# Performance work log

Hardware: AMD Instinct MI355X
Metric: run time of the kernel (lower is better)

Reference implementation:

```python
import jax, jax.numpy as jnp
import numpy as np

GT_POSITIVE_THRESHOLD = 3.0  # pixels, from config['gt_positive_threshold']


def setup_inputs() -> dict:
    key = jax.random.key(0)
    k0, k1, k2 = jax.random.split(key, 3)
    B, N0, N1 = 8, 2048, 2048
    W, H = 640.0, 480.0
    scale = jnp.array([W, H], dtype=jnp.float32)
    kpts0 = jax.random.uniform(k0, (B, N0, 2), dtype=jnp.float32) * scale
    kpts1 = jax.random.uniform(k1, (B, N1, 2), dtype=jnp.float32) * scale
    # near-identity homography per pair (small perturbation keeps points in-frame)
    transformation = (jnp.eye(3, dtype=jnp.float32)[None]
                      + 0.001 * jax.random.normal(k2, (B, 3, 3), dtype=jnp.float32))
    return {"kpts0": kpts0, "kpts1": kpts1, "transformation": transformation}


def _reproject_keypoints(kpts, H):
    # kpts: [B,N,2], H: [B,3,3] homography. Homogeneous projection.
    ones = jnp.ones(kpts.shape[:-1] + (1,), dtype=kpts.dtype)
    pts_h = jnp.concatenate([kpts, ones], axis=-1)           # [B,N,3]
    proj = jnp.einsum('bij,bnj->bni', H, pts_h)              # [B,N,3]
    return proj[..., :2] / (proj[..., 2:3] + 1e-8)


def _cdist(a, b):
    # a: [B,N0,2], b: [B,N1,2] -> [B,N0,N1] Euclidean distances
    a2 = jnp.sum(a * a, axis=-1)                             # [B,N0]
    b2 = jnp.sum(b * b, axis=-1)                             # [B,N1]
    ab = jnp.einsum('bnd,bmd->bnm', a, b)                    # [B,N0,N1]
    d2 = a2[:, :, None] + b2[:, None, :] - 2.0 * ab
    return jnp.sqrt(jnp.maximum(d2, 0.0))


def reference(kpts0, kpts1, transformation):
    B, N0, _ = kpts0.shape
    N1 = kpts1.shape[1]
    kpts0_t = _reproject_keypoints(kpts0, transformation)
    err = _cdist(kpts0_t, kpts1)                             # [B,N0,N1]

    min_dist0 = jnp.min(err, axis=2)                         # [B,N0]
    gt_matches0 = jnp.argmin(err, axis=2).astype(jnp.int32)  # [B,N0]
    gt_matches1 = jnp.argmin(err, axis=1).astype(jnp.int32)  # [B,N1]

    # cross-check: kpts1's best match of kpts0's best match must be the kpt itself
    back = jnp.take_along_axis(gt_matches1, gt_matches0, axis=1)  # [B,N0]
    idx0 = jnp.arange(N0, dtype=jnp.int32)[None, :]
    inconsistent = (back != idx0) | (min_dist0 > GT_POSITIVE_THRESHOLD)
    gt_matches0 = jnp.where(inconsistent, -1, gt_matches0)

    # rebuild inverse map: gt_matches1[b, gt_matches0[b,i]] = i for valid i
    valid = gt_matches0 != -1
    tgt = jnp.where(valid, gt_matches0, N1)                  # N1 is out-of-range -> dropped
    src = jnp.broadcast_to(idx0, (B, N0))
    gt_matches1_out = jnp.full((B, N1), -1, dtype=jnp.int32)
    gt_matches1_out = gt_matches1_out.at[jnp.arange(B)[:, None], tgt].set(src, mode='drop')

    return gt_matches0, gt_matches1_out, min_dist0
```

## Files before the change

### kernel.cpp

```cpp
#include <hip/hip_runtime.h>


#define SPN 2048
#define SPT 16384
#define HGRID (SPT / 16)

__device__ __forceinline__ void sp_reproject(const float* __restrict__ T, int b,
                                             float x, float y,
                                             float& X, float& Y, float& S) {
  const float* H = T + b * 9;
  float p0 = __fadd_rn(__fadd_rn(__fmul_rn(H[0], x), __fmul_rn(H[1], y)), H[2]);
  float p1 = __fadd_rn(__fadd_rn(__fmul_rn(H[3], x), __fmul_rn(H[4], y)), H[5]);
  float p2 = __fadd_rn(__fadd_rn(__fmul_rn(H[6], x), __fmul_rn(H[7], y)), H[8]);
  float den = __fadd_rn(p2, 1e-8f);
  X = __fdiv_rn(p0, den);
  Y = __fdiv_rn(p1, den);
  S = __fadd_rn(__fmul_rn(X, X), __fmul_rn(Y, Y));
}

__global__ __launch_bounds__(256) void sp_prep(
    const float2* __restrict__ k0, const float2* __restrict__ k1,
    const float* __restrict__ T, float4* __restrict__ q0, float4* __restrict__ q1) {
  int t = blockIdx.x * 256 + threadIdx.x;
  if (t < SPT) {
    float2 p = k0[t];
    float X, Y, S;
    sp_reproject(T, t >> 11, p.x, p.y, X, Y, S);
    q0[t] = make_float4(X, Y, S, 0.0f);
  } else {
    int u = t - SPT;
    float2 p = k1[u];
    float S = __fadd_rn(__fmul_rn(p.x, p.x), __fmul_rn(p.y, p.y));
    q1[u] = make_float4(p.x, p.y, S, 0.0f);
  }
}

__global__ __launch_bounds__(256, 4) void SuperPointMatchesGenerator_56925496541369_kernel(
    const float4* __restrict__ q0, const float4* __restrict__ q1,
    unsigned short* __restrict__ gt0p, unsigned short* __restrict__ gt1,
    float* __restrict__ out_mind) {
  __shared__ float4 cand[SPN];
  const int tid = threadIdx.x;
  const bool m1 = blockIdx.x >= HGRID;
  const int base = (m1 ? blockIdx.x - HGRID : blockIdx.x) << 4;
  const int b = base >> 11, cb = b << 11;
  const float4* __restrict__ qr = m1 ? q1 : q0;
  const float4* __restrict__ qc = (m1 ? q0 : q1) + cb;

  float4 stage[8];
#pragma unroll
  for (int k = 0; k < 8; k++) stage[k] = qc[(k << 8) + tid];
#pragma unroll
  for (int k = 0; k < 8; k++) cand[(k << 8) + tid] = stage[k];

  float rx2[16], ry2[16], rsv[16], bv[16];
  int bi[16];
#pragma unroll
  for (int r = 0; r < 16; r++) {
    float4 v = qr[base + r];
    rx2[r] = __fmul_rn(2.0f, v.x);
    ry2[r] = __fmul_rn(2.0f, v.y);
    rsv[r] = v.z;
    bv[r] = INFINITY; bi[r] = 0;
  }
  __syncthreads();

  float4 vv[8];
#pragma unroll
  for (int k = 0; k < 8; k++) vv[k] = cand[(k << 8) + tid];
#pragma unroll
  for (int k = 0; k < 8; k++) {
    const int c = (k << 8) + tid;
#pragma unroll
    for (int r = 0; r < 16; r++) {
      float tw = __fadd_rn(__fmul_rn(rx2[r], vv[k].x), __fmul_rn(ry2[r], vv[k].y));
      float s  = __fadd_rn(rsv[r], vv[k].z);
      float d2 = __fsub_rn(s, tw);
      if (d2 < bv[r]) { bv[r] = d2; bi[r] = c; }
    }
  }
  __syncthreads();

  unsigned long long* keys = (unsigned long long*)cand;
#pragma unroll
  for (int r = 0; r < 16; r++) {
    float dm = fmaxf(bv[r], 0.0f);
    keys[(r << 8) + tid] =
        ((unsigned long long)__float_as_uint(dm) << 32) | (unsigned)bi[r];
  }
  __syncthreads();

  const int wv = tid >> 6, ln = tid & 63;
#pragma unroll
  for (int rr = 0; rr < 4; rr++) {
    const int r = (wv << 2) + rr;
    unsigned long long k0 = keys[(r << 8) + ln];
    unsigned long long t;
    t = keys[(r << 8) + 64 + ln];  if (t < k0) k0 = t;
    t = keys[(r << 8) + 128 + ln]; if (t < k0) k0 = t;
    t = keys[(r << 8) + 192 + ln]; if (t < k0) k0 = t;
#pragma unroll
    for (int off = 32; off > 0; off >>= 1) {
      unsigned long long o = __shfl_down(k0, off);
      if (o < k0) k0 = o;
    }
    if (ln == 0) {
      int idx = (int)(k0 & 0x7ffu);
      if (!m1) {
        float e = __fsqrt_rn(__uint_as_float((unsigned)(k0 >> 32)));
        unsigned short pk = (unsigned short)idx;
        if (e > 3.0f) pk |= 0x8000u;
        gt0p[base + r] = pk;
        out_mind[base + r] = e;
      } else {
        gt1[base + r] = (unsigned short)idx;
      }
    }
  }
}

__global__ __launch_bounds__(256) void SuperPointMatchesGenerator_56925496541369_final(
    const unsigned short* __restrict__ gt0p, const unsigned short* __restrict__ gt1,
    float* __restrict__ out) {
  int t = blockIdx.x * 256 + threadIdx.x;
  if (t >= SPT) return;
  int b = t >> 11, i = t & 2047, cb = b << 11;

  unsigned short p0 = gt0p[t];
  int m0 = p0 & 0x7ff;
  bool ok0 = ((p0 & 0x8000u) == 0) && ((int)gt1[cb + m0] == i);
  out[t] = ok0 ? (float)m0 : -1.0f;

  int istar = gt1[t];
  unsigned short ps = gt0p[cb + istar];
  bool ok1 = (((int)(ps & 0x7ff)) == i) && ((ps & 0x8000u) == 0);
  out[SPT + t] = ok1 ? (float)istar : -1.0f;
}

__global__ __launch_bounds__(256) void sp_fb_main(
    const float2* __restrict__ k0, const float2* __restrict__ k1,
    const float* __restrict__ T, unsigned short* __restrict__ gt0p,
    unsigned short* __restrict__ gt1, float* __restrict__ out_mind) {
  const bool mode1 = blockIdx.x >= SPN;
  const int base = (mode1 ? blockIdx.x - SPN : blockIdx.x) * 8;
  const int b = base >> 11, cb = b << 11;
  float rx[8], ry[8], rs[8], bv[8];
  int bi[8];
#pragma unroll
  for (int r = 0; r < 8; r++) { bv[r] = INFINITY; bi[r] = 0; }
  if (!mode1) {
#pragma unroll
    for (int r = 0; r < 8; r++) {
      float2 p = k0[base + r];
      sp_reproject(T, b, p.x, p.y, rx[r], ry[r], rs[r]);
    }
    for (int c = threadIdx.x; c < SPN; c += 256) {
      float2 p = k1[cb + c];
      float b2 = __fadd_rn(__fmul_rn(p.x, p.x), __fmul_rn(p.y, p.y));
#pragma unroll
      for (int r = 0; r < 8; r++) {
        float ab = __fadd_rn(__fmul_rn(rx[r], p.x), __fmul_rn(ry[r], p.y));
        float d2 = __fsub_rn(__fadd_rn(rs[r], b2), __fmul_rn(2.0f, ab));
        float dm = fmaxf(d2, 0.0f);
        if (dm < bv[r]) { bv[r] = dm; bi[r] = c; }
      }
    }
  } else {
#pragma unroll
    for (int r = 0; r < 8; r++) {
      float2 p = k1[base + r];
      rx[r] = p.x; ry[r] = p.y;
      rs[r] = __fadd_rn(__fmul_rn(p.x, p.x), __fmul_rn(p.y, p.y));
    }
    for (int c = threadIdx.x; c < SPN; c += 256) {
      float2 p = k0[cb + c];
      float cx, cy, a2;
      sp_reproject(T, b, p.x, p.y, cx, cy, a2);
#pragma unroll
      for (int r = 0; r < 8; r++) {
        float ab = __fadd_rn(__fmul_rn(rx[r], cx), __fmul_rn(ry[r], cy));
        float d2 = __fsub_rn(__fadd_rn(a2, rs[r]), __fmul_rn(2.0f, ab));
        float dm = fmaxf(d2, 0.0f);
        if (dm < bv[r]) { bv[r] = dm; bi[r] = c; }
      }
    }
  }
  unsigned long long key[8];
#pragma unroll
  for (int r = 0; r < 8; r++)
    key[r] = ((unsigned long long)__float_as_uint(bv[r]) << 32) | (unsigned)bi[r];
#pragma unroll
  for (int off = 32; off > 0; off >>= 1) {
#pragma unroll
    for (int r = 0; r < 8; r++) {
      unsigned long long o = __shfl_down(key[r], off);
      if (o < key[r]) key[r] = o;
    }
  }
  __shared__ unsigned long long part[4][8];
  if ((threadIdx.x & 63) == 0) {
    int w = threadIdx.x >> 6;
#pragma unroll
    for (int r = 0; r < 8; r++) part[w][r] = key[r];
  }
  __syncthreads();
  if (threadIdx.x < 8) {
    int r = threadIdx.x;
    unsigned long long k = part[0][r];
#pragma unroll
    for (int w = 1; w < 4; w++)
      if (part[w][r] < k) k = part[w][r];
    int idx = (int)(k & 0x7ffu);
    if (!mode1) {
      float e = __fsqrt_rn(__uint_as_float((unsigned)(k >> 32)));
      unsigned short pk = (unsigned short)idx;
      if (e > 3.0f) pk |= 0x8000u;
      gt0p[base + r] = pk;
      out_mind[base + r] = e;
    } else {
      gt1[base + r] = (unsigned short)idx;
    }
  }
}

extern "C" void kernel_launch(void* const* d_in, const int* in_sizes, int n_in,
                              void* d_out, int out_size, void* d_ws, size_t ws_size,
                              hipStream_t stream) {
  (void)in_sizes; (void)n_in; (void)out_size;
  const float2* k0 = (const float2*)d_in[0];
  const float2* k1 = (const float2*)d_in[1];
  const float* T   = (const float*)d_in[2];
  float* out = (float*)d_out;

  const size_t need = (size_t)2 * SPT * sizeof(float4) + (size_t)2 * SPT * sizeof(unsigned short);
  if (ws_size >= need) {
    float4* q0 = (float4*)d_ws;
    float4* q1 = q0 + SPT;
    unsigned short* gt0p = (unsigned short*)(q1 + SPT);
    unsigned short* gt1  = gt0p + SPT;
    sp_prep<<<2 * SPT / 256, 256, 0, stream>>>(k0, k1, T, q0, q1);
    SuperPointMatchesGenerator_56925496541369_kernel<<<2 * HGRID, 256, 0, stream>>>(
        q0, q1, gt0p, gt1, out + 2 * SPT);
    SuperPointMatchesGenerator_56925496541369_final<<<SPT / 256, 256, 0, stream>>>(
        gt0p, gt1, out);
  } else {
    unsigned short* gt0p = (unsigned short*)d_ws;
    unsigned short* gt1  = gt0p + SPT;
    sp_fb_main<<<2 * SPN, 256, 0, stream>>>(k0, k1, T, gt0p, gt1, out + 2 * SPT);
    SuperPointMatchesGenerator_56925496541369_final<<<SPT / 256, 256, 0, stream>>>(
        gt0p, gt1, out);
  }
}
```

Baseline: 79.35 us.

## Fuse prep, argmin and cross-check into one cooperative kernel with grid syncs

Replaces the three-kernel sequence (prep, bidirectional argmin, final cross-check) with a single cooperative kernel of 1024 blocks. Grid-wide syncs separate the phases, and each block handles both directions in turn. The aim is to remove two kernel launch gaps. In exchange it relies on cooperative launch support and the cost of grid.sync, and the grid is half as wide per phase, which may lower parallelism. The multi-kernel path is kept as a fallback, and the old no-workspace path is removed.

```diff
diff --git a/kernel.cpp b/kernel.cpp
--- a/kernel.cpp
+++ b/kernel.cpp
@@ -1,8 +1,12 @@
 #include <hip/hip_runtime.h>
+#include <hip/hip_cooperative_groups.h>
+
+namespace cg = cooperative_groups;
 
 
 #define SPN 2048
 #define SPT 16384
+#define CGRID 1024
 #define HGRID (SPT / 16)
 
 __device__ __forceinline__ void sp_reproject(const float* __restrict__ T, int b,
@@ -16,6 +20,127 @@
   X = __fdiv_rn(p0, den);
   Y = __fdiv_rn(p1, den);
   S = __fadd_rn(__fmul_rn(X, X), __fmul_rn(Y, Y));
+}
+
+__global__ __launch_bounds__(256, 4) void SuperPointMatchesGenerator_56925496541369_kernel(
+    const float2* __restrict__ k0, const float2* __restrict__ k1,
+    const float* __restrict__ T, float4* __restrict__ q0, float4* __restrict__ q1,
+    unsigned short* __restrict__ gt0p, unsigned short* __restrict__ gt1,
+    float* __restrict__ out) {
+  cg::grid_group grid = cg::this_grid();
+  __shared__ float4 cand[SPN + 512];
+  const int tid = threadIdx.x;
+  const int gt = (int)blockIdx.x * 256 + tid;
+  float* __restrict__ out_mind = out + 2 * SPT;
+
+  if (gt < 2 * SPT) {
+    if (gt < SPT) {
+      float2 p = k0[gt];
+      float X, Y, S;
+      sp_reproject(T, gt >> 11, p.x, p.y, X, Y, S);
+      q0[gt] = make_float4(X, Y, S, 0.0f);
+    } else {
+      int u = gt - SPT;
+      float2 p = k1[u];
+      float S = __fadd_rn(__fmul_rn(p.x, p.x), __fmul_rn(p.y, p.y));
+      q1[u] = make_float4(p.x, p.y, S, 0.0f);
+    }
+  }
+  grid.sync();
+
+  for (int half = 0; half < 2; half++) {
+    __syncthreads();
+    const bool m1 = (half == 1);
+    const int base = (int)blockIdx.x << 4;
+    const int b = base >> 11, cb = b << 11;
+    const float4* __restrict__ qr = m1 ? q1 : q0;
+    const float4* __restrict__ qc = (m1 ? q0 : q1) + cb;
+
+    float4 stage[8];
+#pragma unroll
+    for (int k = 0; k < 8; k++) stage[k] = qc[(k << 8) + tid];
+#pragma unroll
+    for (int k = 0; k < 8; k++) cand[(k << 8) + tid] = stage[k];
+
+    float rx2[16], ry2[16], rsv[16], bv[16];
+    int bi[16];
+#pragma unroll
+    for (int r = 0; r < 16; r++) {
+      float4 v = qr[base + r];
+      rx2[r] = __fmul_rn(2.0f, v.x);
+      ry2[r] = __fmul_rn(2.0f, v.y);
+      rsv[r] = v.z;
+      bv[r] = INFINITY; bi[r] = 0;
+    }
+    __syncthreads();
+
+    float4 vv[8];
+#pragma unroll
+    for (int k = 0; k < 8; k++) vv[k] = cand[(k << 8) + tid];
+#pragma unroll
+    for (int k = 0; k < 8; k++) {
+      const int c = (k << 8) + tid;
+#pragma unroll
+      for (int r = 0; r < 16; r++) {
+        float tw = __fadd_rn(__fmul_rn(rx2[r], vv[k].x), __fmul_rn(ry2[r], vv[k].y));
+        float s  = __fadd_rn(rsv[r], vv[k].z);
+        float d2 = __fsub_rn(s, tw);
+        if (d2 < bv[r]) { bv[r] = d2; bi[r] = c; }
+      }
+    }
+    __syncthreads();
+
+    unsigned long long* keys = (unsigned long long*)cand;
+#pragma unroll
+    for (int r = 0; r < 16; r++) {
+      float dm = fmaxf(bv[r], 0.0f);
+      keys[(r << 8) + tid] =
+          ((unsigned long long)__float_as_uint(dm) << 32) | (unsigned)bi[r];
+    }
+    __syncthreads();
+
+    const int wv = tid >> 6, ln = tid & 63;
+#pragma unroll
+    for (int rr = 0; rr < 4; rr++) {
+      const int r = (wv << 2) + rr;
+      unsigned long long kk = keys[(r << 8) + ln];
+      unsigned long long t;
+      t = keys[(r << 8) + 64 + ln];  if (t < kk) kk = t;
+      t = keys[(r << 8) + 128 + ln]; if (t < kk) kk = t;
+      t = keys[(r << 8) + 192 + ln]; if (t < kk) kk = t;
+#pragma unroll
+      for (int off = 32; off > 0; off >>= 1) {
+        unsigned long long o = __shfl_down(kk, off);
+        if (o < kk) kk = o;
+      }
+      if (ln == 0) {
+        int idx = (int)(kk & 0x7ffu);
+        if (!m1) {
+          float e = __fsqrt_rn(__uint_as_float((unsigned)(kk >> 32)));
+          unsigned short pk = (unsigned short)idx;
+          if (e > 3.0f) pk |= 0x8000u;
+          gt0p[base + r] = pk;
+          out_mind[base + r] = e;
+        } else {
+          gt1[base + r] = (unsigned short)idx;
+        }
+      }
+    }
+  }
+  grid.sync();
+
+  if (gt < SPT) {
+    int b2 = gt >> 11, i = gt & 2047, cb2 = b2 << 11;
+    unsigned short p0 = gt0p[gt];
+    int m0i = p0 & 0x7ff;
+    bool ok0 = ((p0 & 0x8000u) == 0) && ((int)gt1[cb2 + m0i] == i);
+    out[gt] = ok0 ? (float)m0i : -1.0f;
+
+    int istar = gt1[gt];
+    unsigned short ps = gt0p[cb2 + istar];
+    bool ok1 = (((int)(ps & 0x7ff)) == i) && ((ps & 0x8000u) == 0);
+    out[SPT + gt] = ok1 ? (float)istar : -1.0f;
+  }
 }
 
 __global__ __launch_bounds__(256) void sp_prep(
@@ -35,7 +160,7 @@
   }
 }
 
-__global__ __launch_bounds__(256, 4) void SuperPointMatchesGenerator_56925496541369_kernel(
+__global__ __launch_bounds__(256, 4) void sp_main3(
     const float4* __restrict__ q0, const float4* __restrict__ q1,
     unsigned short* __restrict__ gt0p, unsigned short* __restrict__ gt1,
     float* __restrict__ out_mind) {
@@ -94,20 +219,20 @@
 #pragma unroll
   for (int rr = 0; rr < 4; rr++) {
     const int r = (wv << 2) + rr;
-    unsigned long long k0 = keys[(r << 8) + ln];
+    unsigned long long kk = keys[(r << 8) + ln];
     unsigned long long t;
-    t = keys[(r << 8) + 64 + ln];  if (t < k0) k0 = t;
-    t = keys[(r << 8) + 128 + ln]; if (t < k0) k0 = t;
-    t = keys[(r << 8) + 192 + ln]; if (t < k0) k0 = t;
+    t = keys[(r << 8) + 64 + ln];  if (t < kk) kk = t;
+    t = keys[(r << 8) + 128 + ln]; if (t < kk) kk = t;
+    t = keys[(r << 8) + 192 + ln]; if (t < kk) kk = t;
 #pragma unroll
     for (int off = 32; off > 0; off >>= 1) {
-      unsigned long long o = __shfl_down(k0, off);
-      if (o < k0) k0 = o;
+      unsigned long long o = __shfl_down(kk, off);
+      if (o < kk) kk = o;
     }
     if (ln == 0) {
-      int idx = (int)(k0 & 0x7ffu);
+      int idx = (int)(kk & 0x7ffu);
       if (!m1) {
-        float e = __fsqrt_rn(__uint_as_float((unsigned)(k0 >> 32)));
+        float e = __fsqrt_rn(__uint_as_float((unsigned)(kk >> 32)));
         unsigned short pk = (unsigned short)idx;
         if (e > 3.0f) pk |= 0x8000u;
         gt0p[base + r] = pk;
@@ -119,7 +244,7 @@
   }
 }
 
-__global__ __launch_bounds__(256) void SuperPointMatchesGenerator_56925496541369_final(
+__global__ __launch_bounds__(256) void sp_final3(
     const unsigned short* __restrict__ gt0p, const unsigned short* __restrict__ gt1,
     float* __restrict__ out) {
   int t = blockIdx.x * 256 + threadIdx.x;
@@ -137,117 +262,42 @@
   out[SPT + t] = ok1 ? (float)istar : -1.0f;
 }
 
-__global__ __launch_bounds__(256) void sp_fb_main(
-    const float2* __restrict__ k0, const float2* __restrict__ k1,
-    const float* __restrict__ T, unsigned short* __restrict__ gt0p,
-    unsigned short* __restrict__ gt1, float* __restrict__ out_mind) {
-  const bool mode1 = blockIdx.x >= SPN;
-  const int base = (mode1 ? blockIdx.x - SPN : blockIdx.x) * 8;
-  const int b = base >> 11, cb = b << 11;
-  float rx[8], ry[8], rs[8], bv[8];
-  int bi[8];
-#pragma unroll
-  for (int r = 0; r < 8; r++) { bv[r] = INFINITY; bi[r] = 0; }
-  if (!mode1) {
-#pragma unroll
-    for (int r = 0; r < 8; r++) {
-      float2 p = k0[base + r];
-      sp_reproject(T, b, p.x, p.y, rx[r], ry[r], rs[r]);
-    }
-    for (int c = threadIdx.x; c < SPN; c += 256) {
-      float2 p = k1[cb + c];
-      float b2 = __fadd_rn(__fmul_rn(p.x, p.x), __fmul_rn(p.y, p.y));
-#pragma unroll
-      for (int r = 0; r < 8; r++) {
-        float ab = __fadd_rn(__fmul_rn(rx[r], p.x), __fmul_rn(ry[r], p.y));
-        float d2 = __fsub_rn(__fadd_rn(rs[r], b2), __fmul_rn(2.0f, ab));
-        float dm = fmaxf(d2, 0.0f);
-        if (dm < bv[r]) { bv[r] = dm; bi[r] = c; }
-      }
-    }
-  } else {
-#pragma unroll
-    for (int r = 0; r < 8; r++) {
-      float2 p = k1[base + r];
-      rx[r] = p.x; ry[r] = p.y;
-      rs[r] = __fadd_rn(__fmul_rn(p.x, p.x), __fmul_rn(p.y, p.y));
-    }
-    for (int c = threadIdx.x; c < SPN; c += 256) {
-      float2 p = k0[cb + c];
-      float cx, cy, a2;
-      sp_reproject(T, b, p.x, p.y, cx, cy, a2);
-#pragma unroll
-      for (int r = 0; r < 8; r++) {
-        float ab = __fadd_rn(__fmul_rn(rx[r], cx), __fmul_rn(ry[r], cy));
-        float d2 = __fsub_rn(__fadd_rn(a2, rs[r]), __fmul_rn(2.0f, ab));
-        float dm = fmaxf(d2, 0.0f);
-        if (dm < bv[r]) { bv[r] = dm; bi[r] = c; }
-      }
-    }
-  }
-  unsigned long long key[8];
-#pragma unroll
-  for (int r = 0; r < 8; r++)
-    key[r] = ((unsigned long long)__float_as_uint(bv[r]) << 32) | (unsigned)bi[r];
-#pragma unroll
-  for (int off = 32; off > 0; off >>= 1) {
-#pragma unroll
-    for (int r = 0; r < 8; r++) {
-      unsigned long long o = __shfl_down(key[r], off);
-      if (o < key[r]) key[r] = o;
-    }
-  }
-  __shared__ unsigned long long part[4][8];
-  if ((threadIdx.x & 63) == 0) {
-    int w = threadIdx.x >> 6;
-#pragma unroll
-    for (int r = 0; r < 8; r++) part[w][r] = key[r];
-  }
-  __syncthreads();
-  if (threadIdx.x < 8) {
-    int r = threadIdx.x;
-    unsigned long long k = part[0][r];
-#pragma unroll
-    for (int w = 1; w < 4; w++)
-      if (part[w][r] < k) k = part[w][r];
-    int idx = (int)(k & 0x7ffu);
-    if (!mode1) {
-      float e = __fsqrt_rn(__uint_as_float((unsigned)(k >> 32)));
-      unsigned short pk = (unsigned short)idx;
-      if (e > 3.0f) pk |= 0x8000u;
-      gt0p[base + r] = pk;
-      out_mind[base + r] = e;
-    } else {
-      gt1[base + r] = (unsigned short)idx;
-    }
-  }
-}
-
 extern "C" void kernel_launch(void* const* d_in, const int* in_sizes, int n_in,
                               void* d_out, int out_size, void* d_ws, size_t ws_size,
                               hipStream_t stream) {
-  (void)in_sizes; (void)n_in; (void)out_size;
+  (void)in_sizes; (void)n_in; (void)out_size; (void)ws_size;
   const float2* k0 = (const float2*)d_in[0];
   const float2* k1 = (const float2*)d_in[1];
   const float* T   = (const float*)d_in[2];
   float* out = (float*)d_out;
 
-  const size_t need = (size_t)2 * SPT * sizeof(float4) + (size_t)2 * SPT * sizeof(unsigned short);
-  if (ws_size >= need) {
-    float4* q0 = (float4*)d_ws;
-    float4* q1 = q0 + SPT;
-    unsigned short* gt0p = (unsigned short*)(q1 + SPT);
-    unsigned short* gt1  = gt0p + SPT;
-    sp_prep<<<2 * SPT / 256, 256, 0, stream>>>(k0, k1, T, q0, q1);
-    SuperPointMatchesGenerator_56925496541369_kernel<<<2 * HGRID, 256, 0, stream>>>(
-        q0, q1, gt0p, gt1, out + 2 * SPT);
-    SuperPointMatchesGenerator_56925496541369_final<<<SPT / 256, 256, 0, stream>>>(
-        gt0p, gt1, out);
-  } else {
-    unsigned short* gt0p = (unsigned short*)d_ws;
-    unsigned short* gt1  = gt0p + SPT;
-    sp_fb_main<<<2 * SPN, 256, 0, stream>>>(k0, k1, T, gt0p, gt1, out + 2 * SPT);
-    SuperPointMatchesGenerator_56925496541369_final<<<SPT / 256, 256, 0, stream>>>(
-        gt0p, gt1, out);
-  }
-}
+  float4* q0 = (float4*)d_ws;
+  float4* q1 = q0 + SPT;
+  unsigned short* gt0p = (unsigned short*)(q1 + SPT);
+  unsigned short* gt1  = gt0p + SPT;
+
+  static int coop_state = -1;
+  if (coop_state < 0) {
+    int dev = 0, attr = 0, ncu = 0, maxb = 0;
+    (void)hipGetDevice(&dev);
+    (void)hipDeviceGetAttribute(&attr, hipDeviceAttributeCooperativeLaunch, dev);
+    (void)hipDeviceGetAttribute(&ncu, hipDeviceAttributeMultiprocessorCount, dev);
+    hipError_t oe = hipOccupancyMaxActiveBlocksPerMultiprocessor(
+        &maxb, SuperPointMatchesGenerator_56925496541369_kernel, 256, 0);
+    coop_state = (attr != 0 && oe == hipSuccess && (long)maxb * ncu >= CGRID) ? 1 : 0;
+  }
+
+  if (coop_state == 1) {
+    void* args[] = {(void*)&k0, (void*)&k1, (void*)&T, (void*)&q0, (void*)&q1,
+                    (void*)&gt0p, (void*)&gt1, (void*)&out};
+    hipError_t le = hipLaunchCooperativeKernel(
+        SuperPointMatchesGenerator_56925496541369_kernel,
+        dim3(CGRID), dim3(256), args, 0, stream);
+    if (le == hipSuccess) return;
+    coop_state = 0;
+  }
+
+  sp_prep<<<2 * SPT / 256, 256, 0, stream>>>(k0, k1, T, q0, q1);
+  sp_main3<<<2 * HGRID, 256, 0, stream>>>(q0, q1, gt0p, gt1, out + 2 * SPT);
+  sp_final3<<<SPT / 256, 256, 0, stream>>>(gt0p, gt1, out);
+}
```

Result: no change. 79.19 us (-0.2%).
